# Kernel tuning notes

Hardware: AMD Instinct MI355X
Metric: run time of the kernel (lower is better)

The kernel has to match this reference:

```python
import jax, jax.numpy as jnp
import numpy as np

B, S, E, H = 2, 2048, 2048, 16
D = E // H  # head_dim = 128


def setup_inputs() -> dict:
    key = jax.random.key(0)
    k1, k2, k3, k4, k5 = jax.random.split(key, 5)
    hidden_states = jax.random.normal(k1, (B, S, E), dtype=jnp.float32)
    # causal mask, broadcastable to attn_shape (B, q, H, k)
    causal = jnp.tril(jnp.ones((S, S), dtype=bool))  # [q, k]
    attention_mask = jnp.broadcast_to(causal[None, :, None, :], (B, S, 1, S))
    c_attn_w = jax.random.normal(k2, (E, E + 2 * D), dtype=jnp.float32) * (E ** -0.5)
    c_attn_b = jax.random.normal(k3, (E + 2 * D,), dtype=jnp.float32) * 0.02
    c_proj_w = jax.random.normal(k4, (E, E), dtype=jnp.float32) * (E ** -0.5)
    c_proj_b = jax.random.normal(k5, (E,), dtype=jnp.float32) * 0.02
    return {
        "hidden_states": hidden_states,
        "attention_mask": attention_mask,
        "c_attn_w": c_attn_w,
        "c_attn_b": c_attn_b,
        "c_proj_w": c_proj_w,
        "c_proj_b": c_proj_b,
    }


def reference(hidden_states, attention_mask, c_attn_w, c_attn_b, c_proj_w, c_proj_b):
    b, s, e = hidden_states.shape
    h, d = H, D
    qkv = hidden_states @ c_attn_w + c_attn_b            # [b, s, e + 2d]
    query = qkv[..., :e]                                 # [b, s, e]
    key = qkv[..., e:e + d]                              # [b, s, d] (single shared KV head)
    value = qkv[..., e + d:]                             # [b, s, d]
    scale = 1.0 / (d ** 0.5)                             # scale_attn_weights, unscale=1
    q = query.reshape(b, s * h, d)
    # QK^T with MQA broadcast: [b, s*h, k]
    scores = jnp.einsum('bqd,bkd->bqk', q, key) * scale
    scores = scores.reshape(b, s, h, s)                  # attn_shape (b, q, h, k)
    mask_value = jnp.finfo(scores.dtype).min
    scores = jnp.where(attention_mask, scores, mask_value)
    probs = jax.nn.softmax(scores, axis=-1)              # fp32 softmax (upcast is no-op in fp32)
    attn = jnp.einsum('bqk,bkd->bqd', probs.reshape(b, s * h, s), value)
    attn = attn.reshape(b, s, e)
    return attn @ c_proj_w + c_proj_b
```

## Files before the change

kernel.cpp:

```cpp
#include <hip/hip_runtime.h>
#include <math.h>


typedef __attribute__((ext_vector_type(8))) short short8;
typedef __attribute__((ext_vector_type(8))) __bf16 bf16x8;
typedef __attribute__((ext_vector_type(4))) float floatx4;
typedef __attribute__((ext_vector_type(4))) unsigned short ushort4v;
typedef __attribute__((ext_vector_type(2))) unsigned uint2v;
typedef unsigned short ushort;

__device__ __forceinline__ ushort f2bf(float f) {
    unsigned u = __builtin_bit_cast(unsigned, f);
    u += 0x7fffu + ((u >> 16) & 1u);
    return (ushort)(u >> 16);
}
__device__ __forceinline__ unsigned pk2(float a, float b) {
    return (unsigned)f2bf(a) | ((unsigned)f2bf(b) << 16);
}

template <typename V>
__device__ __forceinline__ auto mfma_try(V a, V b, floatx4 c, int)
    -> decltype(__builtin_amdgcn_mfma_f32_16x16x32_bf16(a, b, c, 0, 0, 0)) {
    return __builtin_amdgcn_mfma_f32_16x16x32_bf16(a, b, c, 0, 0, 0);
}
template <typename V>
__device__ __forceinline__ floatx4 mfma_try(V a, V b, floatx4 c, long) {
    return __builtin_amdgcn_mfma_f32_16x16x32_bf16(
        __builtin_bit_cast(bf16x8, a), __builtin_bit_cast(bf16x8, b), c, 0, 0, 0);
}
__device__ __forceinline__ floatx4 mfma_bf16(short8 a, short8 b, floatx4 c) {
    return mfma_try(a, b, c, 0);
}

__device__ __forceinline__ void gld_lds16(const ushort* g, ushort* l) {
    __builtin_amdgcn_global_load_lds(
        (const __attribute__((address_space(1))) unsigned*)(const void*)g,
        (__attribute__((address_space(3))) unsigned*)(void*)l, 16, 0, 0);
}

__global__ __launch_bounds__(256) void convert_bf16(const float* __restrict__ X,
                                                    ushort* __restrict__ Y, int n4) {
    int i = blockIdx.x * 256 + threadIdx.x;
    if (i >= n4) return;
    float4 v = ((const float4*)X)[i];
    ushort4v o = {f2bf(v.x), f2bf(v.y), f2bf(v.z), f2bf(v.w)};
    *(ushort4v*)&Y[(size_t)i * 4] = o;
}

__global__ __launch_bounds__(256) void transpose_convert(const float* __restrict__ W,
                                                         ushort* __restrict__ WT,
                                                         int K, int N) {
    __shared__ ushort T[64][68];
    const int tid = threadIdx.x;
    const int n0 = blockIdx.x * 64, k0 = blockIdx.y * 64;
    #pragma unroll
    for (int i = 0; i < 4; ++i) {
        int k = (tid >> 4) + i * 16, n = (tid & 15) * 4;
        float4 v = *(const float4*)&W[(size_t)(k0 + k) * N + n0 + n];
        T[n + 0][k] = f2bf(v.x); T[n + 1][k] = f2bf(v.y);
        T[n + 2][k] = f2bf(v.z); T[n + 3][k] = f2bf(v.w);
    }
    __syncthreads();
    #pragma unroll
    for (int i = 0; i < 4; ++i) {
        int idx = tid + i * 256;
        int n = idx >> 4, c4 = idx & 15;
        *(ushort4v*)&WT[(size_t)(n0 + n) * K + k0 + c4 * 4] =
            *(const ushort4v*)&T[n][c4 * 4];
    }
}

__global__ __launch_bounds__(256) void v_transpose(const ushort* __restrict__ qkv,
                                                   ushort* __restrict__ VTg) {
    __shared__ ushort T[64 * 72];
    const int tid = threadIdx.x;
    const int s0 = blockIdx.x * 64, d0 = blockIdx.y * 64, b = blockIdx.z;
    const size_t bS = (size_t)b * 2048;
    #pragma unroll
    for (int i = 0; i < 2; ++i) {
        int idx = tid + i * 256;
        int s = idx >> 3, d8 = idx & 7;
        short8 v = *(const short8*)&qkv[(bS + s0 + s) * 2304 + 2176 + d0 + d8 * 8];
        #pragma unroll
        for (int j = 0; j < 8; ++j)
            T[(d8 * 8 + j) * 72 + s] = (ushort)v[j];
    }
    __syncthreads();
    #pragma unroll
    for (int i = 0; i < 2; ++i) {
        int idx = tid + i * 256;
        int d = idx >> 3, s8 = idx & 7;
        *(short8*)&VTg[((size_t)b * 128 + d0 + d) * 2048 + s0 + s8 * 8] =
            *(const short8*)&T[d * 72 + s8 * 8];
    }
}

template <int MODE>
__global__ __launch_bounds__(256) void gemm_m97(
    const ushort* __restrict__ A, const ushort* __restrict__ BT,
    const float* __restrict__ bias, void* __restrict__ C, int M, int N, int K)
{
    __shared__ ushort As[8192];
    __shared__ ushort Bs[8192];
    const int tid = threadIdx.x, lane = tid & 63, wid = tid >> 6;
    const int wr = wid >> 1, wc = wid & 1;
    const int lg = lane >> 4, li = lane & 15;
    const int m0 = blockIdx.y * 128, n0 = blockIdx.x * 128;
    const int srow = lane >> 3;
    const int sphys = (lane & 7) * 16;
    floatx4 acc[4][4] = {};

    for (int k0 = 0; k0 < K; k0 += 64) {
        __syncthreads();
        #pragma unroll
        for (int i = 0; i < 4; ++i) {
            const int c = wid * 4 + i;
            const int row = c * 8 + srow;
            const int lin = sphys ^ ((row & 7) << 4);
            gld_lds16(&A[(size_t)(m0 + row) * K + k0 + (lin >> 1)], &As[c * 512]);
            gld_lds16(&BT[(size_t)(n0 + row) * K + k0 + (lin >> 1)], &Bs[c * 512]);
        }
        __syncthreads();
        #pragma unroll
        for (int kk = 0; kk < 2; ++kk) {
            short8 af[4], bfv[4];
            const int pb = (kk * 64 + lg * 16) ^ ((li & 7) << 4);
            #pragma unroll
            for (int m = 0; m < 4; ++m)
                af[m] = *(const short8*)&As[(wr * 64 + m * 16 + li) * 64 + (pb >> 1)];
            #pragma unroll
            for (int n = 0; n < 4; ++n)
                bfv[n] = *(const short8*)&Bs[(wc * 64 + n * 16 + li) * 64 + (pb >> 1)];
            #pragma unroll
            for (int m = 0; m < 4; ++m)
                #pragma unroll
                for (int n = 0; n < 4; ++n)
                    acc[m][n] = mfma_bf16(af[m], bfv[n], acc[m][n]);
        }
    }

    #pragma unroll
    for (int m = 0; m < 4; ++m) {
        #pragma unroll
        for (int n = 0; n < 4; ++n) {
            const int col = n0 + wc * 64 + n * 16 + li;
            const float bv = bias[col];
            #pragma unroll
            for (int r = 0; r < 4; ++r) {
                const int row = m0 + wr * 64 + m * 16 + lg * 4 + r;
                float v = acc[m][n][r] + bv;
                if constexpr (MODE == 0) {
                    if (col < 2048) v *= 0.08838834764831845f;
                    ((ushort*)C)[(size_t)row * N + col] = f2bf(v);
                } else {
                    ((float*)C)[(size_t)row * N + col] = v;
                }
            }
        }
    }
}

#define STAGE_KV(t_, Kdst, Vdst)                                               \
    {                                                                          \
        const int k0_ = (t_) * 64;                                             \
        _Pragma("unroll")                                                      \
        for (int i_ = 0; i_ < 4; ++i_) {                                       \
            const int idx_ = gtid + i_ * 256;                                  \
            const int row_ = idx_ >> 4, g_ = idx_ & 15;                        \
            const int src_ = (g_ * 16) ^ ((row_ & 7) << 4);                    \
            gld_lds16(&qkv[(bS + k0_ + row_) * QKV + E + (src_ >> 1)],         \
                      &(Kdst)[(i_ * 256 + gwid * 64) * 8]);                    \
        }                                                                      \
        _Pragma("unroll")                                                      \
        for (int i_ = 0; i_ < 4; ++i_) {                                       \
            const int idx_ = gtid + i_ * 256;                                  \
            const int d_ = idx_ >> 3, kg_ = idx_ & 7;                          \
            gld_lds16(&VTg[((size_t)b * 128 + d_) * 2048 + k0_ +               \
                           ((kg_ ^ (d_ & 7)) << 3)],                           \
                      &(Vdst)[(i_ * 256 + gwid * 64) * 8]);                    \
        }                                                                      \
    }

__global__ __launch_bounds__(512, 2) void attn_kernel(
    const ushort* __restrict__ qkv,
    const ushort* __restrict__ VTg,
    ushort* __restrict__ out)
{
    constexpr int S = 2048, Dh = 128, QKV = 2304, E = 2048;
    __shared__ ushort lds[81920];
    ushort* Ps = lds + 65536;

    const int tid = threadIdx.x, lane = tid & 63, wid = tid >> 6;
    const int gtid = tid & 255;
    const int grp = wid >> 2, gwid = wid & 3;
    const int lg = lane >> 4, li = lane & 15;
    const int pr = blockIdx.x;
    const int h = blockIdx.y, b = blockIdx.z;
    const size_t bS = (size_t)b * S;

    for (int pass = 0; pass < 2; ++pass) {
        const int st = pass ? (15 - pr) : pr;
        const int qA = st * 128 + gwid * 16;
        const int qB = qA + 64;
        const int niter = st + 1;
        const int tbase = grp * niter;

        short8 qfA[4], qfB[4];
        #pragma unroll
        for (int dc = 0; dc < 4; ++dc) {
            qfA[dc] = *(const short8*)&qkv[(bS + qA + li) * QKV + h * Dh + dc * 32 + lg * 8];
            qfB[dc] = *(const short8*)&qkv[(bS + qB + li) * QKV + h * Dh + dc * 32 + lg * 8];
        }

        floatx4 oA[8] = {}, oB[8] = {};
        float mA = -1e30f, lA = 0.f, mB = -1e30f, lB = 0.f;

        STAGE_KV(tbase, lds + (grp * 2) * 8192, lds + 32768 + (grp * 2) * 8192);

        for (int it = 0; it < niter; ++it) {
            const int t = tbase + it;
            __builtin_amdgcn_s_barrier();
            ushort* Kcur = lds + (grp * 2 + (it & 1)) * 8192;
            ushort* Vcur = lds + 32768 + (grp * 2 + (it & 1)) * 8192;
            if (it + 1 < niter) {
                STAGE_KV(t + 1, lds + (grp * 2 + ((it + 1) & 1)) * 8192,
                         lds + 32768 + (grp * 2 + ((it + 1) & 1)) * 8192);
                asm volatile("s_waitcnt vmcnt(8)" ::: "memory");
            } else {
                asm volatile("s_waitcnt vmcnt(0)" ::: "memory");
            }
            __builtin_amdgcn_sched_barrier(0);
            __builtin_amdgcn_s_barrier();

            floatx4 sA[4] = {{0,0,0,0},{0,0,0,0},{0,0,0,0},{0,0,0,0}};
            floatx4 sB[4] = {{0,0,0,0},{0,0,0,0},{0,0,0,0},{0,0,0,0}};
            __builtin_amdgcn_s_setprio(1);
            #pragma unroll
            for (int dc = 0; dc < 4; ++dc) {
                #pragma unroll
                for (int kb = 0; kb < 4; ++kb) {
                    short8 kf = *(const short8*)&Kcur[(kb * 16 + li) * 128 +
                                                      (((dc * 4 + lg) ^ (li & 7)) << 3)];
                    sA[kb] = mfma_bf16(kf, qfA[dc], sA[kb]);
                    sB[kb] = mfma_bf16(kf, qfB[dc], sB[kb]);
                }
            }
            __builtin_amdgcn_s_setprio(0);

            if (t == 2 * st) {
                #pragma unroll
                for (int kb = 0; kb < 4; ++kb)
                    #pragma unroll
                    for (int r = 0; r < 4; ++r)
                        if (kb * 16 + lg * 4 + r > gwid * 16 + li) sA[kb][r] = -2e30f;
            }
            if (t == 2 * st + 1) {
                #pragma unroll
                for (int kb = 0; kb < 4; ++kb)
                    #pragma unroll
                    for (int r = 0; r < 4; ++r) {
                        sA[kb][r] = -2e30f;
                        if (kb * 16 + lg * 4 + r > gwid * 16 + li) sB[kb][r] = -2e30f;
                    }
            }

            {
                float mt = fmaxf(fmaxf(fmaxf(sA[0][0], sA[0][1]), fmaxf(sA[0][2], sA[0][3])),
                                 fmaxf(fmaxf(sA[1][0], sA[1][1]), fmaxf(sA[1][2], sA[1][3])));
                mt = fmaxf(mt, fmaxf(fmaxf(fmaxf(sA[2][0], sA[2][1]), fmaxf(sA[2][2], sA[2][3])),
                                     fmaxf(fmaxf(sA[3][0], sA[3][1]), fmaxf(sA[3][2], sA[3][3]))));
                mt = fmaxf(mt, __shfl_xor(mt, 16));
                mt = fmaxf(mt, __shfl_xor(mt, 32));
                if (!__all(mt <= mA)) {
                    const float mn = fmaxf(mA, mt);
                    const float sc = __expf(mA - mn);
                    mA = mn;
                    lA *= sc;
                    #pragma unroll
                    for (int db = 0; db < 8; ++db) oA[db] *= sc;
                }
                float rs = 0.f;
                #pragma unroll
                for (int kb = 0; kb < 4; ++kb)
                    #pragma unroll
                    for (int r = 0; r < 4; ++r) {
                        float p = __expf(sA[kb][r] - mA);
                        sA[kb][r] = p; rs += p;
                    }
                rs += __shfl_xor(rs, 16);
                rs += __shfl_xor(rs, 32);
                lA += rs;
                #pragma unroll
                for (int kb = 0; kb < 4; ++kb) {
                    const int g = kb * 2 + (lg >> 1);
                    const int sw = ((g ^ (li & 7)) << 3) + ((lg & 1) * 4);
                    uint2v w = {pk2(sA[kb][0], sA[kb][1]), pk2(sA[kb][2], sA[kb][3])};
                    *(uint2v*)&Ps[wid * 2048 + li * 64 + sw] = w;
                }
            }
            {
                float mt = fmaxf(fmaxf(fmaxf(sB[0][0], sB[0][1]), fmaxf(sB[0][2], sB[0][3])),
                                 fmaxf(fmaxf(sB[1][0], sB[1][1]), fmaxf(sB[1][2], sB[1][3])));
                mt = fmaxf(mt, fmaxf(fmaxf(fmaxf(sB[2][0], sB[2][1]), fmaxf(sB[2][2], sB[2][3])),
                                     fmaxf(fmaxf(sB[3][0], sB[3][1]), fmaxf(sB[3][2], sB[3][3]))));
                mt = fmaxf(mt, __shfl_xor(mt, 16));
                mt = fmaxf(mt, __shfl_xor(mt, 32));
                if (!__all(mt <= mB)) {
                    const float mn = fmaxf(mB, mt);
                    const float sc = __expf(mB - mn);
                    mB = mn;
                    lB *= sc;
                    #pragma unroll
                    for (int db = 0; db < 8; ++db) oB[db] *= sc;
                }
                float rs = 0.f;
                #pragma unroll
                for (int kb = 0; kb < 4; ++kb)
                    #pragma unroll
                    for (int r = 0; r < 4; ++r) {
                        float p = __expf(sB[kb][r] - mB);
                        sB[kb][r] = p; rs += p;
                    }
                rs += __shfl_xor(rs, 16);
                rs += __shfl_xor(rs, 32);
                lB += rs;
                #pragma unroll
                for (int kb = 0; kb < 4; ++kb) {
                    const int g = kb * 2 + (lg >> 1);
                    const int sw = ((g ^ (li & 7)) << 3) + ((lg & 1) * 4);
                    uint2v w = {pk2(sB[kb][0], sB[kb][1]), pk2(sB[kb][2], sB[kb][3])};
                    *(uint2v*)&Ps[wid * 2048 + 1024 + li * 64 + sw] = w;
                }
            }

            __builtin_amdgcn_s_setprio(1);
            #pragma unroll
            for (int kc = 0; kc < 2; ++kc) {
                short8 pA = *(const short8*)&Ps[wid * 2048 + li * 64 +
                                                (((kc * 4 + lg) ^ (li & 7)) << 3)];
                short8 pB = *(const short8*)&Ps[wid * 2048 + 1024 + li * 64 +
                                                (((kc * 4 + lg) ^ (li & 7)) << 3)];
                #pragma unroll
                for (int db = 0; db < 8; ++db) {
                    short8 vt = *(const short8*)&Vcur[(db * 16 + li) * 64 +
                                                      (((kc * 4 + lg) ^ (li & 7)) << 3)];
                    oA[db] = mfma_bf16(vt, pA, oA[db]);
                    oB[db] = mfma_bf16(vt, pB, oB[db]);
                }
            }
            __builtin_amdgcn_s_setprio(0);
        }

        float* fbuf = (float*)lds;
        ushort* Pw = lds + wid * 2176;
        __syncthreads();

        if (grp == 1) {
            float* dst = fbuf + (gwid * 64 + lane) * 36;
            #pragma unroll
            for (int db = 0; db < 8; ++db) *(floatx4*)&dst[db * 4] = oA[db];
            dst[32] = mA; dst[33] = lA;
        }
        __syncthreads();
        if (grp == 0) {
            const float* src = fbuf + (gwid * 64 + lane) * 36;
            const float m1 = src[32], l1 = src[33];
            const float mm = fmaxf(mA, m1);
            const float s0 = __expf(mA - mm), s1 = __expf(m1 - mm);
            #pragma unroll
            for (int db = 0; db < 8; ++db) {
                floatx4 o1 = *(const floatx4*)&src[db * 4];
                oA[db] = oA[db] * s0 + o1 * s1;
            }
            lA = lA * s0 + l1 * s1;
        }
        __syncthreads();
        if (grp == 0) {
            const float inv = 1.0f / lA;
            #pragma unroll
            for (int db = 0; db < 8; ++db) {
                *(unsigned*)&Pw[li * 136 + db * 16 + lg * 4]     = pk2(oA[db][0] * inv, oA[db][1] * inv);
                *(unsigned*)&Pw[li * 136 + db * 16 + lg * 4 + 2] = pk2(oA[db][2] * inv, oA[db][3] * inv);
            }
            #pragma unroll
            for (int i = 0; i < 4; ++i) {
                const int q = lane >> 2, d8 = (lane & 3) + i * 4;
                short8 vv = *(const short8*)&Pw[q * 136 + d8 * 8];
                *(short8*)&out[(bS + qA + q) * E + h * Dh + d8 * 8] = vv;
            }
        }
        __syncthreads();

        if (grp == 1) {
            float* dst = fbuf + (gwid * 64 + lane) * 36;
            #pragma unroll
            for (int db = 0; db < 8; ++db) *(floatx4*)&dst[db * 4] = oB[db];
            dst[32] = mB; dst[33] = lB;
        }
        __syncthreads();
        if (grp == 0) {
            const float* src = fbuf + (gwid * 64 + lane) * 36;
            const float m1 = src[32], l1 = src[33];
            const float mm = fmaxf(mB, m1);
            const float s0 = __expf(mB - mm), s1 = __expf(m1 - mm);
            #pragma unroll
            for (int db = 0; db < 8; ++db) {
                floatx4 o1 = *(const floatx4*)&src[db * 4];
                oB[db] = oB[db] * s0 + o1 * s1;
            }
            lB = lB * s0 + l1 * s1;
        }
        __syncthreads();
        if (grp == 0) {
            const float inv = 1.0f / lB;
            #pragma unroll
            for (int db = 0; db < 8; ++db) {
                *(unsigned*)&Pw[li * 136 + db * 16 + lg * 4]     = pk2(oB[db][0] * inv, oB[db][1] * inv);
                *(unsigned*)&Pw[li * 136 + db * 16 + lg * 4 + 2] = pk2(oB[db][2] * inv, oB[db][3] * inv);
            }
            #pragma unroll
            for (int i = 0; i < 4; ++i) {
                const int q = lane >> 2, d8 = (lane & 3) + i * 4;
                short8 vv = *(const short8*)&Pw[q * 136 + d8 * 8];
                *(short8*)&out[(bS + qB + q) * E + h * Dh + d8 * 8] = vv;
            }
        }
        __syncthreads();
    }
}

extern "C" void kernel_launch(void* const* d_in, const int* in_sizes, int n_in,
                              void* d_out, int out_size, void* d_ws, size_t ws_size,
                              hipStream_t stream) {
    (void)in_sizes; (void)n_in; (void)out_size; (void)ws_size;
    const float* hidden   = (const float*)d_in[0];
    const float* c_attn_w = (const float*)d_in[2];
    const float* c_attn_b = (const float*)d_in[3];
    const float* c_proj_w = (const float*)d_in[4];
    const float* c_proj_b = (const float*)d_in[5];
    float* outp = (float*)d_out;

    char* ws = (char*)d_ws;
    ushort* hbf  = (ushort*)ws;
    ushort* W1T  = (ushort*)(ws + (size_t)16777216);
    ushort* W2T  = (ushort*)(ws + (size_t)16777216 + 9437184);
    ushort* qkv  = (ushort*)(ws + (size_t)16777216 + 9437184 + 8388608);
    ushort* VTg  = (ushort*)(ws + (size_t)16777216 + 9437184 + 8388608 + 18874368);
    ushort* attn = hbf;

    convert_bf16<<<8192, 256, 0, stream>>>(hidden, hbf, 4096 * 2048 / 4);
    transpose_convert<<<dim3(36, 32), 256, 0, stream>>>(c_attn_w, W1T, 2048, 2304);
    transpose_convert<<<dim3(32, 32), 256, 0, stream>>>(c_proj_w, W2T, 2048, 2048);

    gemm_m97<0><<<dim3(18, 32), 256, 0, stream>>>(hbf, W1T, c_attn_b, qkv, 4096, 2304, 2048);
    v_transpose<<<dim3(32, 2, 2), 256, 0, stream>>>(qkv, VTg);
    attn_kernel<<<dim3(8, 16, 2), 512, 0, stream>>>(qkv, VTg, attn);
    gemm_m97<1><<<dim3(16, 32), 256, 0, stream>>>(attn, W2T, c_proj_b, outp, 4096, 2048, 2048);
}
```

Measured before the change: 209.5 us.

## Double-buffer GEMM LDS tiles with async prefetch and swizzled block order

The GEMM kernel now keeps two LDS buffers for A and B and issues the global-to-LDS loads for the next K step before computing on the current one. It waits on partial vmcnt so the loads overlap the MFMA work. It also remaps block IDs in an XCD-aware swizzle to improve L2 locality, and sets launch bounds to two blocks per CU. The cost is double the LDS (64KB per block), which may limit occupancy. The hand-placed waitcnt and barriers must also correctly cover the async LDS writes.

```diff
diff --git a/kernel.cpp b/kernel.cpp
--- a/kernel.cpp
+++ b/kernel.cpp
@@ -95,42 +95,68 @@
     }
 }
 
+#define STAGE_AB(k0_, buf_)                                                    \
+    {                                                                          \
+        _Pragma("unroll")                                                      \
+        for (int i_ = 0; i_ < 4; ++i_) {                                       \
+            const int c_ = wid * 4 + i_;                                       \
+            const int row_ = c_ * 8 + srow;                                    \
+            const int lin_ = sphys ^ ((row_ & 7) << 4);                        \
+            gld_lds16(&Ag[(size_t)(m0 + row_) * K + (k0_) + (lin_ >> 1)],      \
+                      &As[buf_][c_ * 512]);                                    \
+            gld_lds16(&Bg[(size_t)(n0 + row_) * K + (k0_) + (lin_ >> 1)],      \
+                      &Bs[buf_][c_ * 512]);                                    \
+        }                                                                      \
+    }
+
 template <int MODE>
-__global__ __launch_bounds__(256) void gemm_m97(
-    const ushort* __restrict__ A, const ushort* __restrict__ BT,
+__global__ __launch_bounds__(256, 2) void gemm_db(
+    const ushort* __restrict__ Ag, const ushort* __restrict__ Bg,
     const float* __restrict__ bias, void* __restrict__ C, int M, int N, int K)
 {
-    __shared__ ushort As[8192];
-    __shared__ ushort Bs[8192];
+    __shared__ ushort As[2][8192];
+    __shared__ ushort Bs[2][8192];
     const int tid = threadIdx.x, lane = tid & 63, wid = tid >> 6;
     const int wr = wid >> 1, wc = wid & 1;
     const int lg = lane >> 4, li = lane & 15;
-    const int m0 = blockIdx.y * 128, n0 = blockIdx.x * 128;
     const int srow = lane >> 3;
     const int sphys = (lane & 7) * 16;
+
+    const int nbx = gridDim.x;
+    const int nwg = nbx * gridDim.y;
+    const int bid = blockIdx.y * nbx + blockIdx.x;
+    const int swz = (bid & 7) * (nwg >> 3) + (bid >> 3);
+    const int m0 = (swz / nbx) * 128, n0 = (swz % nbx) * 128;
+
     floatx4 acc[4][4] = {};
-
-    for (int k0 = 0; k0 < K; k0 += 64) {
-        __syncthreads();
-        #pragma unroll
-        for (int i = 0; i < 4; ++i) {
-            const int c = wid * 4 + i;
-            const int row = c * 8 + srow;
-            const int lin = sphys ^ ((row & 7) << 4);
-            gld_lds16(&A[(size_t)(m0 + row) * K + k0 + (lin >> 1)], &As[c * 512]);
-            gld_lds16(&BT[(size_t)(n0 + row) * K + k0 + (lin >> 1)], &Bs[c * 512]);
-        }
-        __syncthreads();
+    const int niter = K >> 6;
+
+    STAGE_AB(0, 0);
+
+    for (int it = 0; it < niter; ++it) {
+        __builtin_amdgcn_s_barrier();
+        if (it + 1 < niter) {
+            STAGE_AB((it + 1) * 64, (it + 1) & 1);
+            asm volatile("s_waitcnt vmcnt(8)" ::: "memory");
+        } else {
+            asm volatile("s_waitcnt vmcnt(0)" ::: "memory");
+        }
+        __builtin_amdgcn_sched_barrier(0);
+        __builtin_amdgcn_s_barrier();
+        __builtin_amdgcn_sched_barrier(0);
+
+        const ushort* Ab = As[it & 1];
+        const ushort* Bb = Bs[it & 1];
         #pragma unroll
         for (int kk = 0; kk < 2; ++kk) {
             short8 af[4], bfv[4];
             const int pb = (kk * 64 + lg * 16) ^ ((li & 7) << 4);
             #pragma unroll
             for (int m = 0; m < 4; ++m)
-                af[m] = *(const short8*)&As[(wr * 64 + m * 16 + li) * 64 + (pb >> 1)];
+                af[m] = *(const short8*)&Ab[(wr * 64 + m * 16 + li) * 64 + (pb >> 1)];
             #pragma unroll
             for (int n = 0; n < 4; ++n)
-                bfv[n] = *(const short8*)&Bs[(wc * 64 + n * 16 + li) * 64 + (pb >> 1)];
+                bfv[n] = *(const short8*)&Bb[(wc * 64 + n * 16 + li) * 64 + (pb >> 1)];
             #pragma unroll
             for (int m = 0; m < 4; ++m)
                 #pragma unroll
@@ -452,8 +478,8 @@
     transpose_convert<<<dim3(36, 32), 256, 0, stream>>>(c_attn_w, W1T, 2048, 2304);
     transpose_convert<<<dim3(32, 32), 256, 0, stream>>>(c_proj_w, W2T, 2048, 2048);
 
-    gemm_m97<0><<<dim3(18, 32), 256, 0, stream>>>(hbf, W1T, c_attn_b, qkv, 4096, 2304, 2048);
+    gemm_db<0><<<dim3(18, 32), 256, 0, stream>>>(hbf, W1T, c_attn_b, qkv, 4096, 2304, 2048);
     v_transpose<<<dim3(32, 2, 2), 256, 0, stream>>>(qkv, VTg);
     attn_kernel<<<dim3(8, 16, 2), 512, 0, stream>>>(qkv, VTg, attn);
-    gemm_m97<1><<<dim3(16, 32), 256, 0, stream>>>(attn, W2T, c_proj_b, outp, 4096, 2048, 2048);
-}
+    gemm_db<1><<<dim3(16, 32), 256, 0, stream>>>(attn, W2T, c_proj_b, outp, 4096, 2048, 2048);
+}
```

Measured after the change: 198.0 us. 5.5% less time.
